# Optimization experiments

Measured on AMD Instinct MI355X. Metric: run time of the kernel, lower is better.

## Reference

```python
import jax, jax.numpy as jnp
import numpy as np

B, T, S = 4, 2048, 2048
D, H, DFF = 1024, 16, 4096
HD = D // H
EPS = 1e-5


def layer_norm(x, gamma, beta):
    mean = x.mean(-1, keepdims=True)
    var = ((x - mean) ** 2).mean(-1, keepdims=True)
    return gamma * (x - mean) / jnp.sqrt(var + EPS) + beta


def attn(q, k, v):
    # q: [B,H,Tq,hd], k,v: [B,H,Tk,hd]
    scores = jnp.einsum('bhqd,bhkd->bhqk', q, k) / (HD ** 0.5)
    p = jax.nn.softmax(scores, axis=-1)
    return jnp.einsum('bhqk,bhkd->bhqd', p, v)


def split_heads(x, n_chunks):
    # x: [B,T,n_chunks*D] -> n_chunks tensors [B,H,T,hd] (matches torch reshape/chunk order)
    b, t, _ = x.shape
    x = x.reshape(b, t, H, n_chunks * HD).transpose(0, 2, 1, 3)
    return jnp.split(x, n_chunks, axis=-1)


def merge_heads(x):
    b, h, t, hd = x.shape
    return x.transpose(0, 2, 1, 3).reshape(b, t, h * hd)


def setup_inputs() -> dict:
    key = jax.random.key(0)
    ks = jax.random.split(key, 16)
    s = 0.02
    return {
        'x_enc': jax.random.normal(ks[0], (B, S, D), jnp.float32),
        'x_dec': jax.random.normal(ks[1], (B, T, D), jnp.float32),
        'qkv_w': jax.random.normal(ks[2], (D, 3 * D), jnp.float32) * s,
        'qkv_b': jnp.zeros((3 * D,), jnp.float32),
        'sa_o_w': jax.random.normal(ks[3], (D, D), jnp.float32) * s,
        'sa_o_b': jnp.zeros((D,), jnp.float32),
        'g1': jnp.ones((D,), jnp.float32),
        'be1': jnp.zeros((D,), jnp.float32),
        'q_w': jax.random.normal(ks[4], (D, D), jnp.float32) * s,
        'q_b': jnp.zeros((D,), jnp.float32),
        'kv_w': jax.random.normal(ks[5], (D, 2 * D), jnp.float32) * s,
        'kv_b': jnp.zeros((2 * D,), jnp.float32),
        'ca_o_w': jax.random.normal(ks[6], (D, D), jnp.float32) * s,
        'ca_o_b': jnp.zeros((D,), jnp.float32),
        'g2': jnp.ones((D,), jnp.float32),
        'be2': jnp.zeros((D,), jnp.float32),
        'ff_w1': jax.random.normal(ks[7], (D, DFF), jnp.float32) * s,
        'ff_b1': jnp.zeros((DFF,), jnp.float32),
        'ff_w2': jax.random.normal(ks[8], (DFF, D), jnp.float32) * s,
        'ff_b2': jnp.zeros((D,), jnp.float32),
        'g3': jnp.ones((D,), jnp.float32),
        'be3': jnp.zeros((D,), jnp.float32),
    }


def reference(x_enc, x_dec, qkv_w, qkv_b, sa_o_w, sa_o_b, g1, be1,
              q_w, q_b, kv_w, kv_b, ca_o_w, ca_o_b, g2, be2,
              ff_w1, ff_b1, ff_w2, ff_b2, g3, be3):
    # --- self attention on x_dec (dropout = identity at inference) ---
    qkv = x_dec @ qkv_w + qkv_b                      # [B,T,3D]
    q, k, v = split_heads(qkv, 3)
    sa = merge_heads(attn(q, k, v)) @ sa_o_w + sa_o_b
    res = layer_norm(sa + x_dec, g1, be1)
    # --- cross attention: q from decoder stream, kv from encoder ---
    kv = x_enc @ kv_w + kv_b                         # [B,S,2D]
    kc, vc = split_heads(kv, 2)
    qc, = split_heads(res @ q_w + q_b, 1)
    ca = merge_heads(attn(qc, kc, vc)) @ ca_o_w + ca_o_b
    res2 = layer_norm(ca + res, g2, be2)
    # --- feed forward ---
    ff = jax.nn.relu(res2 @ ff_w1 + ff_b1) @ ff_w2 + ff_b2
    return layer_norm(ff + res2, g3, be3)
```

## Files before the change

### kernel.cpp

```cpp
#include <hip/hip_runtime.h>

typedef unsigned short u16;
typedef unsigned int   u32;
typedef __bf16 bf16_t;
typedef bf16_t bf16x4 __attribute__((ext_vector_type(4)));
typedef bf16_t bf16x8 __attribute__((ext_vector_type(8)));
typedef float  f32x4  __attribute__((ext_vector_type(4)));

__device__ __forceinline__ u16 f2bf(float f) {
  u32 u = __builtin_bit_cast(u32, f);
  u32 r = u + 0x7fffu + ((u >> 16) & 1u);
  return (u16)(r >> 16);
}
__device__ __forceinline__ float bf2f(u16 h) {
  u32 u = ((u32)h) << 16;
  return __builtin_bit_cast(float, u);
}

__device__ __forceinline__ void gl_lds16(const u16* g, u16* l) {
  __builtin_amdgcn_global_load_lds(
      (const __attribute__((address_space(1))) u32*)g,
      (__attribute__((address_space(3))) u32*)l, 16, 0, 0);
}

__global__ __launch_bounds__(256) void k_cvt(const float* __restrict__ in,
                                             u16* __restrict__ out, long n4) {
  long i = (long)blockIdx.x * 256 + threadIdx.x;
  if (i >= n4) return;
  float4 v = reinterpret_cast<const float4*>(in)[i];
  ushort4 o;
  o.x = f2bf(v.x); o.y = f2bf(v.y); o.z = f2bf(v.z); o.w = f2bf(v.w);
  reinterpret_cast<ushort4*>(out)[i] = o;
}

__global__ __launch_bounds__(256) void k_transpose_cvt(const float* __restrict__ W,
                                                       u16* __restrict__ Wt,
                                                       int K, int N) {
  __shared__ u16 tile[32][33];
  int n0 = blockIdx.x * 32, k0 = blockIdx.y * 32;
  int tx = threadIdx.x & 31, ty = threadIdx.x >> 5;
#pragma unroll
  for (int i = 0; i < 4; ++i) {
    int k = ty + i * 8;
    tile[k][tx] = f2bf(W[(size_t)(k0 + k) * N + n0 + tx]);
  }
  __syncthreads();
#pragma unroll
  for (int i = 0; i < 4; ++i) {
    int n = ty + i * 8;
    Wt[(size_t)(n0 + n) * K + k0 + tx] = tile[tx][n];
  }
}

__global__ __launch_bounds__(256) void k_vtrans(const u16* __restrict__ in,
                                                u16* __restrict__ out,
                                                long long ibs, int ihs, int irs,
                                                int Tk) {
  __shared__ u16 t[64][72];
  const int tid = threadIdx.x;
  const int head = blockIdx.y;
  const int b = head >> 4, h = head & 15;
  const int kt = blockIdx.x * 64;
  const u16* ip = in + (size_t)b * ibs + (size_t)h * ihs;
  u16* op = out + (size_t)head * 64 * Tk;
#pragma unroll
  for (int i = 0; i < 2; ++i) {
    int c = i * 256 + tid;
    int key = c >> 3, d = (c & 7) * 8;
    *reinterpret_cast<uint4*>(&t[key][d]) =
        *reinterpret_cast<const uint4*>(ip + (size_t)(kt + key) * irs + d);
  }
  __syncthreads();
#pragma unroll
  for (int i = 0; i < 2; ++i) {
    int c = i * 256 + tid;
    int d = c >> 3, k8 = (c & 7) * 8;
    ushort4 lo, hi;
    lo.x = t[k8 + 0][d]; lo.y = t[k8 + 1][d]; lo.z = t[k8 + 2][d]; lo.w = t[k8 + 3][d];
    hi.x = t[k8 + 4][d]; hi.y = t[k8 + 5][d]; hi.z = t[k8 + 6][d]; hi.w = t[k8 + 7][d];
    uint4 o;
    o.x = ((u32)lo.y << 16) | lo.x; o.y = ((u32)lo.w << 16) | lo.z;
    o.z = ((u32)hi.y << 16) | hi.x; o.w = ((u32)hi.w << 16) | hi.z;
    *reinterpret_cast<uint4*>(op + (size_t)d * Tk + kt + k8) = o;
  }
}

template<int RELU>
__global__ __launch_bounds__(256) void k_gemm_bt(
    const u16* __restrict__ A, const u16* __restrict__ Bt,
    const float* __restrict__ bias, u16* __restrict__ C,
    int M, int N, int K)
{
  __shared__ __align__(16) u16 As[2][128 * 64];
  __shared__ __align__(16) u16 Bs[2][128 * 64];
  const int tid = threadIdx.x;
  const int lane = tid & 63, wid = tid >> 6;
  const int wr = wid >> 1, wc = wid & 1;
  const int l15 = lane & 15, g = lane >> 4;
  const int bm = blockIdx.x * 128, bn = blockIdx.y * 128;
  const int srow = lane >> 3, scol = (lane & 7) * 8;

  f32x4 acc[4][4] = {};

  auto stage = [&](int buf, int kt) {
#pragma unroll
    for (int i = 0; i < 4; ++i) {
      int ch = wid * 4 + i;
      gl_lds16(A  + (size_t)(bm + ch * 8 + srow) * K + kt + scol, &As[buf][ch * 512]);
      gl_lds16(Bt + (size_t)(bn + ch * 8 + srow) * K + kt + scol, &Bs[buf][ch * 512]);
    }
  };

  stage(0, 0);
  __syncthreads();
  int cur = 0;
  for (int kt = 0; kt < K; kt += 64) {
    if (kt + 64 < K) stage(cur ^ 1, kt + 64);
#pragma unroll
    for (int ks = 0; ks < 2; ++ks) {
      bf16x8 af[4], bfr[4];
#pragma unroll
      for (int m = 0; m < 4; ++m)
        af[m] = *reinterpret_cast<const bf16x8*>(&As[cur][(wr * 64 + m * 16 + l15) * 64 + ks * 32 + g * 8]);
#pragma unroll
      for (int n = 0; n < 4; ++n)
        bfr[n] = *reinterpret_cast<const bf16x8*>(&Bs[cur][(wc * 64 + n * 16 + l15) * 64 + ks * 32 + g * 8]);
      __builtin_amdgcn_s_setprio(1);
#pragma unroll
      for (int m = 0; m < 4; ++m)
#pragma unroll
        for (int n = 0; n < 4; ++n)
          acc[m][n] = __builtin_amdgcn_mfma_f32_16x16x32_bf16(af[m], bfr[n], acc[m][n], 0, 0, 0);
      __builtin_amdgcn_s_setprio(0);
    }
    __syncthreads();
    cur ^= 1;
  }
#pragma unroll
  for (int n = 0; n < 4; ++n) {
    int col = bn + wc * 64 + n * 16 + l15;
    float bv = bias[col];
#pragma unroll
    for (int m = 0; m < 4; ++m) {
      int row0 = bm + wr * 64 + m * 16 + g * 4;
#pragma unroll
      for (int r = 0; r < 4; ++r) {
        float v = acc[m][n][r] + bv;
        if (RELU) v = fmaxf(v, 0.f);
        C[(size_t)(row0 + r) * N + col] = f2bf(v);
      }
    }
  }
}

template<int RELU>
__global__ __launch_bounds__(512, 1) void k_gemm256(
    const u16* __restrict__ A, const u16* __restrict__ Bt,
    const float* __restrict__ bias, u16* __restrict__ C,
    int M, int N, int K)
{
  __shared__ __align__(16) u16 lds[65536];
  const int tid = threadIdx.x;
  const int lane = tid & 63, wid = tid >> 6;
  const int wr = wid >> 2, wc = wid & 3;
  const int l15 = lane & 15, g = lane >> 4;
  const int bm = blockIdx.x * 256, bn = blockIdx.y * 256;
  const int srow = tid >> 3;
  const int swcol = (((tid & 7) ^ ((tid >> 3) & 7)) * 8);
  const int swr = l15 & 7;

  f32x4 acc[8][4] = {};

  auto stageA = [&](int buf, int j, int kt) {
    gl_lds16(A + (size_t)(bm + j * 64 + srow) * K + kt + swcol,
             lds + buf * 32768 + j * 4096 + wid * 512);
  };
  auto stageB = [&](int buf, int j, int kt) {
    gl_lds16(Bt + (size_t)(bn + j * 64 + srow) * K + kt + swcol,
             lds + buf * 32768 + 16384 + j * 4096 + wid * 512);
  };

  stageB(0, 0, 0); stageB(0, 1, 0); stageB(0, 2, 0); stageB(0, 3, 0);
  stageA(0, 0, 0); stageA(0, 2, 0); stageA(0, 1, 0); stageA(0, 3, 0);
  asm volatile("s_waitcnt vmcnt(2)" ::: "memory");
  __builtin_amdgcn_s_barrier();

  int cur = 0;
  for (int kt = 0; kt < K; kt += 64) {
    const u16* Ab = lds + cur * 32768;
    const u16* Bb = lds + cur * 32768 + 16384;
    const bool pre = (kt + 64 < K);
    const int nb = cur ^ 1;
    bf16x8 af[4][2], bflo[2][2], bfhi[2][2];

#pragma unroll
    for (int m = 0; m < 4; ++m)
#pragma unroll
      for (int ks = 0; ks < 2; ++ks)
        af[m][ks] = *reinterpret_cast<const bf16x8*>(
            &Ab[(2 * wr) * 4096 + (m * 16 + l15) * 64 + (((ks * 4 + g) ^ swr) * 8)]);
#pragma unroll
    for (int n = 0; n < 2; ++n)
#pragma unroll
      for (int ks = 0; ks < 2; ++ks)
        bflo[n][ks] = *reinterpret_cast<const bf16x8*>(
            &Bb[wc * 4096 + (n * 16 + l15) * 64 + (((ks * 4 + g) ^ swr) * 8)]);
    if (pre) { stageB(nb, 0, kt + 64); stageB(nb, 1, kt + 64); }
    __builtin_amdgcn_s_setprio(1);
#pragma unroll
    for (int m = 0; m < 4; ++m)
#pragma unroll
      for (int n = 0; n < 2; ++n)
#pragma unroll
        for (int ks = 0; ks < 2; ++ks)
          acc[m][n] = __builtin_amdgcn_mfma_f32_16x16x32_bf16(af[m][ks], bflo[n][ks], acc[m][n], 0, 0, 0);
    __builtin_amdgcn_s_setprio(0);
    __builtin_amdgcn_s_barrier();

#pragma unroll
    for (int n = 0; n < 2; ++n)
#pragma unroll
      for (int ks = 0; ks < 2; ++ks)
        bfhi[n][ks] = *reinterpret_cast<const bf16x8*>(
            &Bb[wc * 4096 + ((n + 2) * 16 + l15) * 64 + (((ks * 4 + g) ^ swr) * 8)]);
    if (pre) { stageB(nb, 2, kt + 64); stageB(nb, 3, kt + 64); }
    __builtin_amdgcn_s_setprio(1);
#pragma unroll
    for (int m = 0; m < 4; ++m)
#pragma unroll
      for (int n = 0; n < 2; ++n)
#pragma unroll
        for (int ks = 0; ks < 2; ++ks)
          acc[m][n + 2] = __builtin_amdgcn_mfma_f32_16x16x32_bf16(af[m][ks], bfhi[n][ks], acc[m][n + 2], 0, 0, 0);
    __builtin_amdgcn_s_setprio(0);
    if (pre) { asm volatile("s_waitcnt vmcnt(4)" ::: "memory"); }
    else     { asm volatile("s_waitcnt vmcnt(0)" ::: "memory"); }
    __builtin_amdgcn_s_barrier();

#pragma unroll
    for (int m = 0; m < 4; ++m)
#pragma unroll
      for (int ks = 0; ks < 2; ++ks)
        af[m][ks] = *reinterpret_cast<const bf16x8*>(
            &Ab[(2 * wr + 1) * 4096 + (m * 16 + l15) * 64 + (((ks * 4 + g) ^ swr) * 8)]);
    if (pre) { stageA(nb, 0, kt + 64); stageA(nb, 2, kt + 64); }
    __builtin_amdgcn_s_setprio(1);
#pragma unroll
    for (int m = 0; m < 4; ++m)
#pragma unroll
      for (int n = 0; n < 2; ++n)
#pragma unroll
        for (int ks = 0; ks < 2; ++ks)
          acc[m + 4][n + 2] = __builtin_amdgcn_mfma_f32_16x16x32_bf16(af[m][ks], bfhi[n][ks], acc[m + 4][n + 2], 0, 0, 0);
    __builtin_amdgcn_s_setprio(0);
    __builtin_amdgcn_s_barrier();

    if (pre) { stageA(nb, 1, kt + 64); stageA(nb, 3, kt + 64); }
    __builtin_amdgcn_s_setprio(1);
#pragma unroll
    for (int m = 0; m < 4; ++m)
#pragma unroll
      for (int n = 0; n < 2; ++n)
#pragma unroll
        for (int ks = 0; ks < 2; ++ks)
          acc[m + 4][n] = __builtin_amdgcn_mfma_f32_16x16x32_bf16(af[m][ks], bflo[n][ks], acc[m + 4][n], 0, 0, 0);
    __builtin_amdgcn_s_setprio(0);
    asm volatile("s_waitcnt vmcnt(2)" ::: "memory");
    __builtin_amdgcn_s_barrier();
    cur ^= 1;
  }

#pragma unroll
  for (int n = 0; n < 4; ++n) {
    int col = bn + wc * 64 + n * 16 + l15;
    float bv = bias[col];
#pragma unroll
    for (int m = 0; m < 8; ++m) {
      int row0 = bm + wr * 128 + m * 16 + g * 4;
#pragma unroll
      for (int r = 0; r < 4; ++r) {
        float v = acc[m][n][r] + bv;
        if (RELU) v = fmaxf(v, 0.f);
        C[(size_t)(row0 + r) * N + col] = f2bf(v);
      }
    }
  }
}

__global__ __launch_bounds__(256) void k_flash2(
    const u16* __restrict__ Qg, const u16* __restrict__ Kg, const u16* __restrict__ VTg,
    u16* __restrict__ Og,
    long long qbs, int qhs, int qrs,
    long long kbs, int khs, int krs,
    long long obs, int ohs, int ors,
    int Tk)
{
  __shared__ __align__(16) u16 Ks[64][72];
  __shared__ __align__(16) u16 Vs[64][72];
  __shared__ __align__(16) u16 Ps[4][16][72];
  const int tid = threadIdx.x;
  const int lane = tid & 63, wid = tid >> 6;
  const int l15 = lane & 15, g = lane >> 4;
  const int head = blockIdx.x;
  const int b = head >> 4, h = head & 15;
  const int srow = tid >> 3, scol = (tid & 7) * 8;

  const u16* Q  = Qg + (size_t)b * qbs + (size_t)h * qhs;
  const u16* Kp = Kg + (size_t)b * kbs + (size_t)h * khs;
  const u16* Vp = VTg + (size_t)head * 64 * Tk;
  u16* Op = Og + (size_t)b * obs + (size_t)h * ohs;

  const int q0 = blockIdx.y * 64 + wid * 16;
  const float SCL = 0.125f * 1.44269504f;

  bf16x8 qf[2];
#pragma unroll
  for (int ks = 0; ks < 2; ++ks)
    qf[ks] = *reinterpret_cast<const bf16x8*>(Q + (size_t)(q0 + l15) * qrs + ks * 32 + g * 8);

  f32x4 oacc[4] = {};
  float lp = 0.f;

  uint4 ka0, ka1, va0, va1, kb0, kb1, vb0, vb1;

  auto load_set = [&](int kt, uint4& k0, uint4& k1, uint4& v0, uint4& v1) {
    k0 = *reinterpret_cast<const uint4*>(Kp + (size_t)(kt + srow) * krs + scol);
    k1 = *reinterpret_cast<const uint4*>(Kp + (size_t)(kt + srow + 32) * krs + scol);
    v0 = *reinterpret_cast<const uint4*>(Vp + (size_t)srow * Tk + kt + scol);
    v1 = *reinterpret_cast<const uint4*>(Vp + (size_t)(srow + 32) * Tk + kt + scol);
  };

  auto tile = [&](const uint4& k0, const uint4& k1, const uint4& v0, const uint4& v1,
                  int ktn, uint4& nk0, uint4& nk1, uint4& nv0, uint4& nv1) {
    __syncthreads();
    *reinterpret_cast<uint4*>(&Ks[srow][scol])      = k0;
    *reinterpret_cast<uint4*>(&Ks[srow + 32][scol]) = k1;
    *reinterpret_cast<uint4*>(&Vs[srow][scol])      = v0;
    *reinterpret_cast<uint4*>(&Vs[srow + 32][scol]) = v1;
    load_set(ktn, nk0, nk1, nv0, nv1);
    __syncthreads();

    f32x4 sc[4] = {};
    __builtin_amdgcn_s_setprio(1);
#pragma unroll
    for (int ks = 0; ks < 2; ++ks)
#pragma unroll
      for (int kb = 0; kb < 4; ++kb) {
        bf16x8 kf = *reinterpret_cast<const bf16x8*>(&Ks[kb * 16 + l15][ks * 32 + g * 8]);
        sc[kb] = __builtin_amdgcn_mfma_f32_16x16x32_bf16(kf, qf[ks], sc[kb], 0, 0, 0);
      }
    __builtin_amdgcn_s_setprio(0);

#pragma unroll
    for (int kb = 0; kb < 4; ++kb) {
      bf16x4 pk;
#pragma unroll
      for (int r = 0; r < 4; ++r) {
        float e = __builtin_amdgcn_exp2f(sc[kb][r] * SCL);
        lp += e;
        pk[r] = (bf16_t)e;
      }
      *reinterpret_cast<bf16x4*>(&Ps[wid][l15][kb * 16 + g * 4]) = pk;
    }
    asm volatile("s_waitcnt lgkmcnt(0)" ::: "memory");
#pragma unroll
    for (int kc = 0; kc < 2; ++kc) {
      bf16x8 pf = *reinterpret_cast<const bf16x8*>(&Ps[wid][l15][kc * 32 + g * 8]);
      __builtin_amdgcn_s_setprio(1);
#pragma unroll
      for (int nb = 0; nb < 4; ++nb) {
        bf16x8 vf = *reinterpret_cast<const bf16x8*>(&Vs[nb * 16 + l15][kc * 32 + g * 8]);
        oacc[nb] = __builtin_amdgcn_mfma_f32_16x16x32_bf16(pf, vf, oacc[nb], 0, 0, 0);
      }
      __builtin_amdgcn_s_setprio(0);
    }
  };

  load_set(0, ka0, ka1, va0, va1);
  for (int kt = 0; kt < Tk; kt += 128) {
    tile(ka0, ka1, va0, va1, kt + 64, kb0, kb1, vb0, vb1);
    int ktn = (kt + 128 < Tk) ? kt + 128 : 0;
    tile(kb0, kb1, vb0, vb1, ktn, ka0, ka1, va0, va1);
  }

  lp += __shfl_xor(lp, 16);
  lp += __shfl_xor(lp, 32);
#pragma unroll
  for (int r = 0; r < 4; ++r) {
    float lr = __shfl(lp, 20 * g + r);
    float inv = 1.f / lr;
#pragma unroll
    for (int nb = 0; nb < 4; ++nb)
      Op[(size_t)(q0 + g * 4 + r) * ors + nb * 16 + l15] = f2bf(oacc[nb][r] * inv);
  }
}

__device__ __forceinline__ void load4v(const float* p, float* v) {
  float4 t = *reinterpret_cast<const float4*>(p);
  v[0] = t.x; v[1] = t.y; v[2] = t.z; v[3] = t.w;
}
__device__ __forceinline__ void load4v(const u16* p, float* v) {
  ushort4 t = *reinterpret_cast<const ushort4*>(p);
  v[0] = bf2f(t.x); v[1] = bf2f(t.y); v[2] = bf2f(t.z); v[3] = bf2f(t.w);
}
__device__ __forceinline__ void store4v(float* p, const float* v) {
  float4 t; t.x = v[0]; t.y = v[1]; t.z = v[2]; t.w = v[3];
  *reinterpret_cast<float4*>(p) = t;
}
__device__ __forceinline__ void store4v(u16* p, const float* v) {
  ushort4 t; t.x = f2bf(v[0]); t.y = f2bf(v[1]); t.z = f2bf(v[2]); t.w = f2bf(v[3]);
  *reinterpret_cast<ushort4*>(p) = t;
}

template<typename TRES, typename TOUT>
__global__ __launch_bounds__(256) void k_add_ln(
    const u16* __restrict__ X, const TRES* __restrict__ R,
    const float* __restrict__ gamma, const float* __restrict__ beta,
    TOUT* __restrict__ Out)
{
  const int row = blockIdx.x;
  const int tid = threadIdx.x;
  const size_t base = (size_t)row * 1024 + tid * 4;
  float x[4], rr[4];
  load4v(X + base, x);
  load4v(R + base, rr);
  float v[4];
#pragma unroll
  for (int j = 0; j < 4; ++j) v[j] = x[j] + rr[j];
  float s = v[0] + v[1] + v[2] + v[3];
  float q = v[0]*v[0] + v[1]*v[1] + v[2]*v[2] + v[3]*v[3];
#pragma unroll
  for (int off = 32; off > 0; off >>= 1) {
    s += __shfl_down(s, off);
    q += __shfl_down(q, off);
  }
  __shared__ float sh[8];
  const int lane = tid & 63, wid = tid >> 6;
  if (lane == 0) { sh[wid] = s; sh[4 + wid] = q; }
  __syncthreads();
  s = sh[0] + sh[1] + sh[2] + sh[3];
  q = sh[4] + sh[5] + sh[6] + sh[7];
  float mean = s * (1.f / 1024.f);
  float var = q * (1.f / 1024.f) - mean * mean;
  float inv = 1.f / sqrtf(var + 1e-5f);
  float gv[4], bv[4], o[4];
  load4v(gamma + tid * 4, gv);
  load4v(beta + tid * 4, bv);
#pragma unroll
  for (int j = 0; j < 4; ++j) o[j] = gv[j] * (v[j] - mean) * inv + bv[j];
  store4v(Out + base, o);
}

extern "C" void kernel_launch(void* const* d_in, const int* in_sizes, int n_in,
                              void* d_out, int out_size, void* d_ws, size_t ws_size,
                              hipStream_t stream)
{
  (void)in_sizes; (void)n_in; (void)out_size; (void)ws_size;
  const float* x_enc  = (const float*)d_in[0];
  const float* x_dec  = (const float*)d_in[1];
  const float* qkv_w  = (const float*)d_in[2];
  const float* qkv_b  = (const float*)d_in[3];
  const float* sa_o_w = (const float*)d_in[4];
  const float* sa_o_b = (const float*)d_in[5];
  const float* g1     = (const float*)d_in[6];
  const float* be1    = (const float*)d_in[7];
  const float* q_w    = (const float*)d_in[8];
  const float* q_b    = (const float*)d_in[9];
  const float* kv_w   = (const float*)d_in[10];
  const float* kv_b   = (const float*)d_in[11];
  const float* ca_o_w = (const float*)d_in[12];
  const float* ca_o_b = (const float*)d_in[13];
  const float* g2     = (const float*)d_in[14];
  const float* be2    = (const float*)d_in[15];
  const float* ff_w1  = (const float*)d_in[16];
  const float* ff_b1  = (const float*)d_in[17];
  const float* ff_w2  = (const float*)d_in[18];
  const float* ff_b2  = (const float*)d_in[19];
  const float* g3     = (const float*)d_in[20];
  const float* be3    = (const float*)d_in[21];
  float* out = (float*)d_out;

  u16* Wb = (u16*)d_ws;
  const size_t O_WQKV = 0;
  const size_t O_WSAO = O_WQKV + (size_t)3072 * 1024;
  const size_t O_WQ   = O_WSAO + (size_t)1024 * 1024;
  const size_t O_WKV  = O_WQ   + (size_t)1024 * 1024;
  const size_t O_WCAO = O_WKV  + (size_t)2048 * 1024;
  const size_t O_WFF1 = O_WCAO + (size_t)1024 * 1024;
  const size_t O_WFF2 = O_WFF1 + (size_t)4096 * 1024;
  const size_t O_XD   = O_WFF2 + (size_t)1024 * 4096;
  const size_t O_XE   = O_XD + 8388608;
  const size_t O_QKV  = O_XE + 8388608;
  const size_t O_QC   = O_QKV + 16777216;
  const size_t O_ATT  = O_QKV + 25165824;
  const size_t O_RES  = O_ATT + 8388608;
  const size_t O_RES2 = O_RES + 8388608;
  const size_t O_FF1  = O_RES2 + 8388608;
  const size_t O_VT   = O_FF1;
  const size_t O_VT2  = O_FF1 + 8388608;
  const size_t O_GO   = O_FF1 + 33554432;

  k_cvt<<<8192, 256, 0, stream>>>(x_dec, Wb + O_XD, 2097152);
  k_cvt<<<8192, 256, 0, stream>>>(x_enc, Wb + O_XE, 2097152);
  k_transpose_cvt<<<dim3(96, 32),  256, 0, stream>>>(qkv_w,  Wb + O_WQKV, 1024, 3072);
  k_transpose_cvt<<<dim3(32, 32),  256, 0, stream>>>(sa_o_w, Wb + O_WSAO, 1024, 1024);
  k_transpose_cvt<<<dim3(32, 32),  256, 0, stream>>>(q_w,    Wb + O_WQ,   1024, 1024);
  k_transpose_cvt<<<dim3(64, 32),  256, 0, stream>>>(kv_w,   Wb + O_WKV,  1024, 2048);
  k_transpose_cvt<<<dim3(32, 32),  256, 0, stream>>>(ca_o_w, Wb + O_WCAO, 1024, 1024);
  k_transpose_cvt<<<dim3(128, 32), 256, 0, stream>>>(ff_w1,  Wb + O_WFF1, 1024, 4096);
  k_transpose_cvt<<<dim3(32, 128), 256, 0, stream>>>(ff_w2,  Wb + O_WFF2, 4096, 1024);

  k_gemm256<0><<<dim3(32, 12), 512, 0, stream>>>(Wb + O_XD, Wb + O_WQKV, qkv_b,
                                                 Wb + O_QKV, 8192, 3072, 1024);
  k_vtrans<<<dim3(32, 64), 256, 0, stream>>>(Wb + O_QKV + 128, Wb + O_VT,
                                             (long long)2048 * 3072, 192, 3072, 2048);
  k_flash2<<<dim3(64, 32), 256, 0, stream>>>(Wb + O_QKV, Wb + O_QKV + 64, Wb + O_VT,
                                             Wb + O_ATT,
                                             (long long)2048 * 3072, 192, 3072,
                                             (long long)2048 * 3072, 192, 3072,
                                             (long long)2048 * 1024, 64, 1024, 2048);
  k_gemm_bt<0><<<dim3(64, 8), 256, 0, stream>>>(Wb + O_ATT, Wb + O_WSAO, sa_o_b,
                                                Wb + O_GO, 8192, 1024, 1024);
  k_add_ln<float, u16><<<8192, 256, 0, stream>>>(Wb + O_GO, x_dec, g1, be1, Wb + O_RES);

  k_gemm256<0><<<dim3(32, 8), 512, 0, stream>>>(Wb + O_XE, Wb + O_WKV, kv_b,
                                                Wb + O_QKV, 8192, 2048, 1024);
  k_vtrans<<<dim3(32, 64), 256, 0, stream>>>(Wb + O_QKV + 64, Wb + O_VT2,
                                             (long long)2048 * 2048, 128, 2048, 2048);
  k_gemm_bt<0><<<dim3(64, 8), 256, 0, stream>>>(Wb + O_RES, Wb + O_WQ, q_b,
                                                Wb + O_QC, 8192, 1024, 1024);
  k_flash2<<<dim3(64, 32), 256, 0, stream>>>(Wb + O_QC, Wb + O_QKV, Wb + O_VT2,
                                             Wb + O_ATT,
                                             (long long)2048 * 1024, 64, 1024,
                                             (long long)2048 * 2048, 128, 2048,
                                             (long long)2048 * 1024, 64, 1024, 2048);
  k_gemm_bt<0><<<dim3(64, 8), 256, 0, stream>>>(Wb + O_ATT, Wb + O_WCAO, ca_o_b,
                                                Wb + O_GO, 8192, 1024, 1024);
  k_add_ln<u16, u16><<<8192, 256, 0, stream>>>(Wb + O_GO, Wb + O_RES, g2, be2, Wb + O_RES2);

  k_gemm256<1><<<dim3(32, 16), 512, 0, stream>>>(Wb + O_RES2, Wb + O_WFF1, ff_b1,
                                                 Wb + O_FF1, 8192, 4096, 1024);
  k_gemm_bt<0><<<dim3(64, 8), 256, 0, stream>>>(Wb + O_FF1, Wb + O_WFF2, ff_b2,
                                                Wb + O_GO, 8192, 1024, 4096);
  k_add_ln<u16, float><<<8192, 256, 0, stream>>>(Wb + O_GO, Wb + O_RES2, g3, be3, out);
}
```

Before: 710.3 us.

## Process two 16-row query tiles per wave in flash attention to reuse K/V

Each wave in the attention kernel now handles 32 query rows instead of 16, so every K and V fragment read from LDS feeds two MFMAs. The block covers 128 query rows, and the grid is halved, which cuts global K/V traffic and barrier overhead per query. The softmax scale is folded into Q at load time, and the row sums are split across two accumulators to shorten the dependency chain. In exchange, register pressure and LDS use rise, occupancy may drop, there are fewer blocks in the grid, and rounding the pre-scaled Q to bf16 adds error.

New measurement: 667.8 us. 6.0% less time.

```diff
diff --git a/kernel.cpp b/kernel.cpp
--- a/kernel.cpp
+++ b/kernel.cpp
@@ -297,7 +297,8 @@
 {
   __shared__ __align__(16) u16 Ks[64][72];
   __shared__ __align__(16) u16 Vs[64][72];
-  __shared__ __align__(16) u16 Ps[4][16][72];
+  __shared__ __align__(16) u16 Ps0[4][16][72];
+  __shared__ __align__(16) u16 Ps1[4][16][72];
   const int tid = threadIdx.x;
   const int lane = tid & 63, wid = tid >> 6;
   const int l15 = lane & 15, g = lane >> 4;
@@ -310,16 +311,23 @@
   const u16* Vp = VTg + (size_t)head * 64 * Tk;
   u16* Op = Og + (size_t)b * obs + (size_t)h * ohs;
 
-  const int q0 = blockIdx.y * 64 + wid * 16;
+  const int q0 = blockIdx.y * 128 + wid * 32;
   const float SCL = 0.125f * 1.44269504f;
 
-  bf16x8 qf[2];
-#pragma unroll
-  for (int ks = 0; ks < 2; ++ks)
-    qf[ks] = *reinterpret_cast<const bf16x8*>(Q + (size_t)(q0 + l15) * qrs + ks * 32 + g * 8);
-
-  f32x4 oacc[4] = {};
-  float lp = 0.f;
+  bf16x8 qf0[2], qf1[2];
+#pragma unroll
+  for (int ks = 0; ks < 2; ++ks) {
+    bf16x8 r0 = *reinterpret_cast<const bf16x8*>(Q + (size_t)(q0 + l15) * qrs + ks * 32 + g * 8);
+    bf16x8 r1 = *reinterpret_cast<const bf16x8*>(Q + (size_t)(q0 + 16 + l15) * qrs + ks * 32 + g * 8);
+#pragma unroll
+    for (int j = 0; j < 8; ++j) {
+      qf0[ks][j] = (bf16_t)((float)r0[j] * SCL);
+      qf1[ks][j] = (bf16_t)((float)r1[j] * SCL);
+    }
+  }
+
+  f32x4 oacc0[4] = {}, oacc1[4] = {};
+  float lp0a = 0.f, lp0b = 0.f, lp1a = 0.f, lp1b = 0.f;
 
   uint4 ka0, ka1, va0, va1, kb0, kb1, vb0, vb1;
 
@@ -340,37 +348,43 @@
     load_set(ktn, nk0, nk1, nv0, nv1);
     __syncthreads();
 
-    f32x4 sc[4] = {};
+    f32x4 sc0[4] = {}, sc1[4] = {};
     __builtin_amdgcn_s_setprio(1);
 #pragma unroll
     for (int ks = 0; ks < 2; ++ks)
 #pragma unroll
       for (int kb = 0; kb < 4; ++kb) {
         bf16x8 kf = *reinterpret_cast<const bf16x8*>(&Ks[kb * 16 + l15][ks * 32 + g * 8]);
-        sc[kb] = __builtin_amdgcn_mfma_f32_16x16x32_bf16(kf, qf[ks], sc[kb], 0, 0, 0);
+        sc0[kb] = __builtin_amdgcn_mfma_f32_16x16x32_bf16(kf, qf0[ks], sc0[kb], 0, 0, 0);
+        sc1[kb] = __builtin_amdgcn_mfma_f32_16x16x32_bf16(kf, qf1[ks], sc1[kb], 0, 0, 0);
       }
     __builtin_amdgcn_s_setprio(0);
 
 #pragma unroll
     for (int kb = 0; kb < 4; ++kb) {
-      bf16x4 pk;
+      bf16x4 pk0, pk1;
 #pragma unroll
       for (int r = 0; r < 4; ++r) {
-        float e = __builtin_amdgcn_exp2f(sc[kb][r] * SCL);
-        lp += e;
-        pk[r] = (bf16_t)e;
+        float e0 = __builtin_amdgcn_exp2f(sc0[kb][r]);
+        float e1 = __builtin_amdgcn_exp2f(sc1[kb][r]);
+        if (kb & 1) { lp0b += e0; lp1b += e1; } else { lp0a += e0; lp1a += e1; }
+        pk0[r] = (bf16_t)e0;
+        pk1[r] = (bf16_t)e1;
       }
-      *reinterpret_cast<bf16x4*>(&Ps[wid][l15][kb * 16 + g * 4]) = pk;
+      *reinterpret_cast<bf16x4*>(&Ps0[wid][l15][kb * 16 + g * 4]) = pk0;
+      *reinterpret_cast<bf16x4*>(&Ps1[wid][l15][kb * 16 + g * 4]) = pk1;
     }
     asm volatile("s_waitcnt lgkmcnt(0)" ::: "memory");
 #pragma unroll
     for (int kc = 0; kc < 2; ++kc) {
-      bf16x8 pf = *reinterpret_cast<const bf16x8*>(&Ps[wid][l15][kc * 32 + g * 8]);
+      bf16x8 pf0 = *reinterpret_cast<const bf16x8*>(&Ps0[wid][l15][kc * 32 + g * 8]);
+      bf16x8 pf1 = *reinterpret_cast<const bf16x8*>(&Ps1[wid][l15][kc * 32 + g * 8]);
       __builtin_amdgcn_s_setprio(1);
 #pragma unroll
       for (int nb = 0; nb < 4; ++nb) {
         bf16x8 vf = *reinterpret_cast<const bf16x8*>(&Vs[nb * 16 + l15][kc * 32 + g * 8]);
-        oacc[nb] = __builtin_amdgcn_mfma_f32_16x16x32_bf16(pf, vf, oacc[nb], 0, 0, 0);
+        oacc0[nb] = __builtin_amdgcn_mfma_f32_16x16x32_bf16(pf0, vf, oacc0[nb], 0, 0, 0);
+        oacc1[nb] = __builtin_amdgcn_mfma_f32_16x16x32_bf16(pf1, vf, oacc1[nb], 0, 0, 0);
       }
       __builtin_amdgcn_s_setprio(0);
     }
@@ -383,15 +397,19 @@
     tile(kb0, kb1, vb0, vb1, ktn, ka0, ka1, va0, va1);
   }
 
-  lp += __shfl_xor(lp, 16);
-  lp += __shfl_xor(lp, 32);
+  float lp0 = lp0a + lp0b;
+  float lp1 = lp1a + lp1b;
+  lp0 += __shfl_xor(lp0, 16); lp0 += __shfl_xor(lp0, 32);
+  lp1 += __shfl_xor(lp1, 16); lp1 += __shfl_xor(lp1, 32);
 #pragma unroll
   for (int r = 0; r < 4; ++r) {
-    float lr = __shfl(lp, 20 * g + r);
-    float inv = 1.f / lr;
-#pragma unroll
-    for (int nb = 0; nb < 4; ++nb)
-      Op[(size_t)(q0 + g * 4 + r) * ors + nb * 16 + l15] = f2bf(oacc[nb][r] * inv);
+    float inv0 = 1.f / __shfl(lp0, 20 * g + r);
+    float inv1 = 1.f / __shfl(lp1, 20 * g + r);
+#pragma unroll
+    for (int nb = 0; nb < 4; ++nb) {
+      Op[(size_t)(q0 + g * 4 + r) * ors + nb * 16 + l15]      = f2bf(oacc0[nb][r] * inv0);
+      Op[(size_t)(q0 + 16 + g * 4 + r) * ors + nb * 16 + l15] = f2bf(oacc1[nb][r] * inv1);
+    }
   }
 }
 
@@ -514,7 +532,7 @@
                                                  Wb + O_QKV, 8192, 3072, 1024);
   k_vtrans<<<dim3(32, 64), 256, 0, stream>>>(Wb + O_QKV + 128, Wb + O_VT,
                                              (long long)2048 * 3072, 192, 3072, 2048);
-  k_flash2<<<dim3(64, 32), 256, 0, stream>>>(Wb + O_QKV, Wb + O_QKV + 64, Wb + O_VT,
+  k_flash2<<<dim3(64, 16), 256, 0, stream>>>(Wb + O_QKV, Wb + O_QKV + 64, Wb + O_VT,
                                              Wb + O_ATT,
                                              (long long)2048 * 3072, 192, 3072,
                                              (long long)2048 * 3072, 192, 3072,
@@ -529,7 +547,7 @@
                                              (long long)2048 * 2048, 128, 2048, 2048);
   k_gemm_bt<0><<<dim3(64, 8), 256, 0, stream>>>(Wb + O_RES, Wb + O_WQ, q_b,
                                                 Wb + O_QC, 8192, 1024, 1024);
-  k_flash2<<<dim3(64, 32), 256, 0, stream>>>(Wb + O_QC, Wb + O_QKV, Wb + O_VT2,
+  k_flash2<<<dim3(64, 16), 256, 0, stream>>>(Wb + O_QC, Wb + O_QKV, Wb + O_VT2,
                                              Wb + O_ATT,
                                              (long long)2048 * 1024, 64, 1024,
                                              (long long)2048 * 2048, 128, 2048,
```
